# Kernel optimization log

Hardware: AMD Instinct MI355X
Metric: run time of the kernel (lower is better)

## Reference

```python
import jax, jax.numpy as jnp
import numpy as np

IN_FEATURES = 1024
OUT_FEATURES = 1024
GRID_SIZE = 5
SPLINE_ORDER = 3
GRID_RANGE = (-1.0, 1.0)


def make_grid():
    h = (GRID_RANGE[1] - GRID_RANGE[0]) / GRID_SIZE
    g = jnp.arange(-SPLINE_ORDER, GRID_SIZE + SPLINE_ORDER + 1, dtype=jnp.float32) * h + GRID_RANGE[0]
    return jnp.tile(g[None, :], (IN_FEATURES, 1))  # (in, G + 2k + 1)


def b_splines(x, grid):
    # x: (N, in), grid: (in, G+2k+1) -> bases: (N, in, G+k)
    xe = x[..., None]
    bases = ((xe >= grid[:, :-1]) & (xe < grid[:, 1:])).astype(x.dtype)
    for k in range(1, SPLINE_ORDER + 1):
        left = (xe - grid[:, :-(k + 1)]) / (grid[:, k:-1] - grid[:, :-(k + 1)])
        right = (grid[:, k + 1:] - xe) / (grid[:, k + 1:] - grid[:, 1:-k])
        bases = left * bases[:, :, :-1] + right * bases[:, :, 1:]
    return bases


def setup_inputs() -> dict:
    key = jax.random.key(0)
    k1, k2, k3 = jax.random.split(key, 3)
    x = jax.random.uniform(k1, (8192, IN_FEATURES), dtype=jnp.float32)
    # lecun_normal-style init: std = 1/sqrt(fan_in)
    base_weight = jax.random.normal(k2, (OUT_FEATURES, IN_FEATURES), dtype=jnp.float32) / np.sqrt(IN_FEATURES)
    coeff = GRID_SIZE + SPLINE_ORDER
    spline_weight = jax.random.normal(k3, (OUT_FEATURES, IN_FEATURES, coeff), dtype=jnp.float32) / np.sqrt(IN_FEATURES * coeff)
    spline_scaler = jnp.ones((OUT_FEATURES, IN_FEATURES), dtype=jnp.float32)
    grid = make_grid()
    return {"x": x, "grid": grid, "base_weight": base_weight,
            "spline_weight": spline_weight, "spline_scaler": spline_scaler}


def reference(x, grid, base_weight, spline_weight, spline_scaler):
    N = x.shape[0]
    base_out = jax.nn.silu(x) @ base_weight.T  # (N, out)
    bases = b_splines(x, grid)                 # (N, in, G+k)
    scaled_sw = spline_weight * spline_scaler[..., None]  # (out, in, G+k)
    spline_out = bases.reshape(N, -1) @ scaled_sw.reshape(OUT_FEATURES, -1).T  # (N, out)
    return base_out + spline_out
```

## Files before the change

### kernel.cpp

```cpp
#include <hip/hip_runtime.h>
#include <hip/hip_bf16.h>

#define IN_F 1024
#define OUT_F 1024
#define KTOT (IN_F * 9)
#define M_ROWS 8192

#define BK 64
#define NT (KTOT / BK)
#define NT_H (NT / 2)

#define A_TILE_E 16384
#define B_TILE_E 8192

typedef short bf16x8 __attribute__((ext_vector_type(8)));
typedef int   i32x4  __attribute__((ext_vector_type(4)));
typedef float f32x4  __attribute__((ext_vector_type(4)));

#define AS1 __attribute__((address_space(1)))
#define AS3 __attribute__((address_space(3)))

__device__ __forceinline__ void kan_basis_fast(
    float xv, const float* __restrict__ g,
    const float* __restrict__ inv1, const float* __restrict__ inv2,
    const float* __restrict__ inv3, float* __restrict__ out) {
  float b[11];
#pragma unroll
  for (int j = 0; j < 11; ++j)
    b[j] = (xv >= g[j] && xv < g[j + 1]) ? 1.0f : 0.0f;
#pragma unroll
  for (int j = 0; j < 10; ++j)
    b[j] = (xv - g[j]) * inv1[j] * b[j] + (g[j + 2] - xv) * inv1[j + 1] * b[j + 1];
#pragma unroll
  for (int j = 0; j < 9; ++j)
    b[j] = (xv - g[j]) * inv2[j] * b[j] + (g[j + 3] - xv) * inv2[j + 1] * b[j + 1];
#pragma unroll
  for (int j = 0; j < 8; ++j)
    b[j] = (xv - g[j]) * inv3[j] * b[j] + (g[j + 4] - xv) * inv3[j + 1] * b[j + 1];
#pragma unroll
  for (int j = 0; j < 8; ++j) out[j] = b[j];
}

__global__ __launch_bounds__(256) void expand_a(
    const float* __restrict__ x, const float* __restrict__ grid,
    __hip_bfloat16* __restrict__ A, int row0, int nrows) {
  const int tid = threadIdx.x;
  const int lane = tid & 63;
  const int wvx = tid >> 6;
  const int l15 = lane & 15;
  const int lhi = lane >> 4;

  const int nb = blockIdx.x >> 3;
  const int ib = blockIdx.x & 7;
  const int n_l = nb * 16 + l15;
  const int i0 = ib * 128 + wvx * 32 + lhi * 8;

  const int bm = n_l >> 8, wm = (n_l >> 6) & 3, m = (n_l >> 4) & 3;

  float g[12];
  const float* gp = grid + (size_t)i0 * 12;
#pragma unroll
  for (int j = 0; j < 12; ++j) g[j] = gp[j];
  float inv1[11], inv2[10], inv3[9];
#pragma unroll
  for (int j = 0; j < 11; ++j) inv1[j] = 1.0f / (g[j + 1] - g[j]);
#pragma unroll
  for (int j = 0; j < 10; ++j) inv2[j] = 1.0f / (g[j + 2] - g[j]);
#pragma unroll
  for (int j = 0; j < 9; ++j)  inv3[j] = 1.0f / (g[j + 3] - g[j]);

  const float* xp = x + (size_t)(row0 + n_l) * IN_F + i0;
  float xs[8];
  *(f32x4*)&xs[0] = *(const f32x4*)xp;
  *(f32x4*)&xs[4] = *(const f32x4*)(xp + 4);

  bf16x8 out[9];
#pragma unroll
  for (int j = 0; j < 8; ++j) {
    float xv = xs[j];
    float bas[8];
    kan_basis_fast(xv, g, inv1, inv2, inv3, bas);
    float s = xv / (1.0f + __expf(-xv));
    out[0][j] = (short)__bfloat16_as_ushort(__float2bfloat16(s));
#pragma unroll
    for (int c = 0; c < 8; ++c)
      out[c + 1][j] = (short)__bfloat16_as_ushort(__float2bfloat16(bas[c]));
  }

#pragma unroll
  for (int c = 0; c < 9; ++c) {
    int k0 = c * IN_F + i0;
    int kt = k0 >> 6;
    int kk = (k0 >> 5) & 1;
    size_t frag = ((((size_t)bm * NT + kt) * 4 + wm) * 4 + m) * 2 + kk;
    *(bf16x8*)(A + frag * 512 + lane * 8) = out[c];
  }
}

__global__ __launch_bounds__(256) void pack_b(
    const float* __restrict__ bw, const float* __restrict__ sw,
    const float* __restrict__ sc, __hip_bfloat16* __restrict__ B) {
  const int tid = threadIdx.x;
  const int lane = tid & 63;
  const int wid = blockIdx.x * 4 + (tid >> 6);
  const int og = wid >> 5;
  const int ib32 = wid & 31;
  const int obn = og >> 3, colg = og & 7;
  const int l15 = lane & 15, lhi = lane >> 4;
  const int o = og * 16 + l15;
  const int i0 = ib32 * 32 + lhi * 8;

  float bwv[8], scv[8];
  const float* bp = bw + (size_t)o * IN_F + i0;
  const float* sp = sc + (size_t)o * IN_F + i0;
  *(f32x4*)&bwv[0] = *(const f32x4*)bp;
  *(f32x4*)&bwv[4] = *(const f32x4*)(bp + 4);
  *(f32x4*)&scv[0] = *(const f32x4*)sp;
  *(f32x4*)&scv[4] = *(const f32x4*)(sp + 4);

  bf16x8 out[9];
#pragma unroll
  for (int j = 0; j < 8; ++j) {
    out[0][j] = (short)__bfloat16_as_ushort(__float2bfloat16(bwv[j]));
    const float* swp = sw + ((size_t)o * IN_F + i0 + j) * 8;
    float swv[8];
    *(f32x4*)&swv[0] = *(const f32x4*)swp;
    *(f32x4*)&swv[4] = *(const f32x4*)(swp + 4);
#pragma unroll
    for (int c = 0; c < 8; ++c)
      out[c + 1][j] = (short)__bfloat16_as_ushort(__float2bfloat16(swv[c] * scv[j]));
  }

#pragma unroll
  for (int c = 0; c < 9; ++c) {
    int kt = c * 16 + (ib32 >> 1);
    int kk = ib32 & 1;
    size_t frag = ((size_t)obn * NT + kt) * 16 + colg * 2 + kk;
    *(bf16x8*)(B + frag * 512 + lane * 8) = out[c];
  }
}


__device__ __forceinline__ void gld16(const __hip_bfloat16* g, __hip_bfloat16* l) {
  __builtin_amdgcn_global_load_lds((AS1 void*)g, (AS3 void*)l, 16, 0, 0);
}

#define DSRO(dst, addr, IMM)                                               \
  asm volatile("ds_read_b128 %0, %1 offset:" #IMM : "=v"(dst) : "v"(addr))

#define SB __builtin_amdgcn_sched_barrier(0)

#define SLOT_E 32768
#define SLOT_B 65536

#define READ_A_KK0(d, aA) do {                                             \
    DSRO(d[0], aA, 0);     DSRO(d[1], aA, 2048);                           \
    DSRO(d[2], aA, 4096);  DSRO(d[3], aA, 6144);                           \
    DSRO(d[4], aA, 8192);  DSRO(d[5], aA, 10240);                          \
    DSRO(d[6], aA, 12288); DSRO(d[7], aA, 14336);                          \
  } while (0)
#define READ_A_KK1(d, aA) do {                                             \
    DSRO(d[0], aA, 1024);  DSRO(d[1], aA, 3072);                           \
    DSRO(d[2], aA, 5120);  DSRO(d[3], aA, 7168);                           \
    DSRO(d[4], aA, 9216);  DSRO(d[5], aA, 11264);                          \
    DSRO(d[6], aA, 13312); DSRO(d[7], aA, 15360);                          \
  } while (0)
#define READ_B_KK0(d, bA) do {                                             \
    DSRO(d[0], bA, 0);     DSRO(d[1], bA, 2048);                           \
    DSRO(d[2], bA, 4096);  DSRO(d[3], bA, 6144);                           \
  } while (0)
#define READ_B_KK1(d, bA) do {                                             \
    DSRO(d[0], bA, 1024);  DSRO(d[1], bA, 3072);                           \
    DSRO(d[2], bA, 5120);  DSRO(d[3], bA, 7168);                           \
  } while (0)

#define MFMA_B(sA, sB) do {                                                \
    __builtin_amdgcn_s_setprio(1);                                         \
    _Pragma("unroll")                                                      \
    for (int m_ = 0; m_ < 8; ++m_)                                         \
      _Pragma("unroll")                                                    \
      for (int n_ = 0; n_ < 4; ++n_)                                       \
        acc[m_][n_] = __builtin_amdgcn_mfma_f32_16x16x32_bf16(             \
            sA[m_], sB[n_], acc[m_][n_], 0, 0, 0);                         \
    __builtin_amdgcn_s_setprio(0);                                         \
  } while (0)

#define STAGE12(DST) do {                                                  \
    gld16(aGp,          (DST) + dstE);                                     \
    gld16(aGp + 4096,   (DST) + dstE + 4096);                              \
    gld16(aGp + 8192,   (DST) + dstE + 8192);                              \
    gld16(aGp + 12288,  (DST) + dstE + 12288);                             \
    gld16(bGp0,         (DST) + dstE + 16384);                             \
    gld16(bGp0 + 4096,  (DST) + dstE + 20480);                             \
    gld16(bGp1,         (DST) + dstE + 24576);                             \
    gld16(bGp1 + 4096,  (DST) + dstE + 28672);                             \
    aGp += 16384; bGp0 += 8192; bGp1 += 8192;                              \
  } while (0)

#define TILE_V12(cA, cB, nA, nB, STAGE_, READN_) do {                      \
    READ_A_KK1(ga, cA); READ_B_KK1(gb, cB);                   \
    STAGE_                                                                 \
    SB;                                                                    \
    asm volatile("s_waitcnt lgkmcnt(12)" ::: "memory"); SB;                \
    MFMA_B(fa, fb);                                                        \
    SB;                                                                    \
    asm volatile("s_waitcnt lgkmcnt(0)" ::: "memory"); SB;                 \
    asm volatile("s_waitcnt vmcnt(0)" ::: "memory"); SB;                   \
    __builtin_amdgcn_s_barrier(); SB;               \
    READN_                                                                 \
    SB;                                                                    \
    MFMA_B(ga, gb);                                                        \
    SB;                                                                    \
  } while (0)

#define READN12(nA, nB) READ_A_KK0(fa, nA); READ_B_KK0(fb, nB);

__global__ __launch_bounds__(512, 2) void gemm_v12(
    const __hip_bfloat16* __restrict__ A, const __hip_bfloat16* __restrict__ B,
    float* __restrict__ C) {
  __shared__ __align__(16) __hip_bfloat16 S[2][SLOT_E];

  const int nwg = gridDim.x;
  const int q = nwg >> 3;
  const int L = (blockIdx.x & 7) * q + (blockIdx.x >> 3);
  const int bm = L >> 3;
  const int khalf = (L >> 2) & 1;
  const int bn2 = L & 3;

  const int tid = threadIdx.x;
  const int lane = tid & 63;
  const int wv = tid >> 6;
  const int wm = wv >> 2;
  const int wn = wv & 3;
  const int l15 = lane & 15, lhi = lane >> 4;

  const int laneE = (wv * 64 + lane) * 8;
  const __hip_bfloat16* aGp =
      A + ((size_t)bm * NT + khalf * NT_H) * A_TILE_E + laneE;
  const __hip_bfloat16* bGp0 =
      B + ((size_t)(2 * bn2) * NT + khalf * NT_H) * B_TILE_E + laneE;
  const __hip_bfloat16* bGp1 =
      B + ((size_t)(2 * bn2 + 1) * NT + khalf * NT_H) * B_TILE_E + laneE;
  __hip_bfloat16* ldsP = &S[0][0];
  const int dstE = wv * 512;

  const uint32_t ldsB = (uint32_t)(uintptr_t)(AS3 const void*)&S[0][0];
  const uint32_t aA0 = ldsB + wm * 16384 + lane * 16;
  const uint32_t aA1 = aA0 + SLOT_B;
  const uint32_t bA0 = ldsB + 32768 + (wn >> 1) * 16384 + (wn & 1) * 8192 + lane * 16;
  const uint32_t bA1 = bA0 + SLOT_B;

  f32x4 acc[8][4];
#pragma unroll
  for (int m = 0; m < 8; ++m)
#pragma unroll
    for (int n = 0; n < 4; ++n) acc[m][n] = f32x4{0.f, 0.f, 0.f, 0.f};

  bf16x8 fa[8], fb[4];
  bf16x8 ga[8], gb[4];

  STAGE12(ldsP);
  asm volatile("s_waitcnt vmcnt(0)" ::: "memory");
  SB;
  __builtin_amdgcn_s_barrier();
  SB;
  READ_A_KK0(fa, aA0); READ_B_KK0(fb, bA0);
  SB;

#pragma unroll 1
  for (int tt = 0; tt < (NT_H - 2) / 2; ++tt) {
    TILE_V12(aA0, bA0, aA1, bA1, STAGE12(ldsP + SLOT_E);, READN12(aA1, bA1));
    TILE_V12(aA1, bA1, aA0, bA0, STAGE12(ldsP);,          READN12(aA0, bA0));
  }
  TILE_V12(aA0, bA0, aA1, bA1, STAGE12(ldsP + SLOT_E);, READN12(aA1, bA1));
  TILE_V12(aA1, bA1, aA0, bA0, ;, ;);

#pragma unroll
  for (int m = 0; m < 8; ++m)
#pragma unroll
    for (int n = 0; n < 4; ++n) {
      int col = bn2 * 256 + (wn >> 1) * 128 + (wn & 1) * 64 + n * 16 + l15;
      int row0 = bm * 256 + wm * 128 + m * 16 + lhi * 4;
#pragma unroll
      for (int j = 0; j < 4; ++j)
        atomicAdd(&C[(size_t)(row0 + j) * OUT_F + col], acc[m][n][j]);
    }
}

__global__ __launch_bounds__(256) void kan_naive(
    const float* __restrict__ x, const float* __restrict__ grid,
    const float* __restrict__ bw, const float* __restrict__ sw,
    const float* __restrict__ sc, float* __restrict__ out) {
  __shared__ float s_act[IN_F];
  __shared__ float s_bas[IN_F * 8];
  int n = blockIdx.x;
  for (int i = threadIdx.x; i < IN_F; i += 256) {
    float xv = x[(size_t)n * IN_F + i];
    float g[12];
    const float* gp = grid + i * 12;
#pragma unroll
    for (int t = 0; t < 12; ++t) g[t] = gp[t];
    float b[11];
#pragma unroll
    for (int j = 0; j < 11; ++j)
      b[j] = (xv >= g[j] && xv < g[j + 1]) ? 1.0f : 0.0f;
#pragma unroll
    for (int k = 1; k <= 3; ++k)
#pragma unroll
      for (int j = 0; j < 11 - k; ++j) {
        float left = (xv - g[j]) / (g[j + k] - g[j]);
        float right = (g[j + k + 1] - xv) / (g[j + k + 1] - g[j + 1]);
        b[j] = left * b[j] + right * b[j + 1];
      }
    s_act[i] = xv / (1.0f + __expf(-xv));
#pragma unroll
    for (int c = 0; c < 8; ++c) s_bas[i * 8 + c] = b[c];
  }
  __syncthreads();
  for (int o = threadIdx.x; o < OUT_F; o += 256) {
    float acc = 0.f;
    const float* bwo = bw + (size_t)o * IN_F;
    const float* swo = sw + (size_t)o * IN_F * 8;
    const float* sco = sc + (size_t)o * IN_F;
    for (int i = 0; i < IN_F; ++i) {
      acc += s_act[i] * bwo[i];
      float p = 0.f;
#pragma unroll
      for (int c = 0; c < 8; ++c) p += s_bas[i * 8 + c] * swo[i * 8 + c];
      acc += p * sco[i];
    }
    out[(size_t)n * OUT_F + o] = acc;
  }
}

extern "C" void kernel_launch(void* const* d_in, const int* in_sizes, int n_in,
                              void* d_out, int out_size, void* d_ws, size_t ws_size,
                              hipStream_t stream) {
  const float* x  = (const float*)d_in[0];
  const float* grid = (const float*)d_in[1];
  const float* bw = (const float*)d_in[2];
  const float* sw = (const float*)d_in[3];
  const float* sc = (const float*)d_in[4];
  float* out = (float*)d_out;

  const size_t Bbytes = (size_t)OUT_F * KTOT * 2;
  const size_t rowBytes = (size_t)KTOT * 2;

  if (ws_size >= Bbytes + 256 * rowBytes) {
    __hip_bfloat16* Bp = (__hip_bfloat16*)d_ws;
    __hip_bfloat16* Ap = (__hip_bfloat16*)((char*)d_ws + Bbytes);
    size_t arows = (ws_size - Bbytes) / rowBytes;
    int chunk = (int)((arows / 256) * 256);
    if (chunk > M_ROWS) chunk = M_ROWS;

    hipMemsetAsync(d_out, 0, (size_t)out_size * sizeof(float), stream);
    pack_b<<<OUT_F * 128 / 256, 256, 0, stream>>>(bw, sw, sc, Bp);
    for (int r0 = 0; r0 < M_ROWS; r0 += chunk) {
      int rows = M_ROWS - r0 < chunk ? M_ROWS - r0 : chunk;
      expand_a<<<(rows / 16) * 8, 256, 0, stream>>>(x, grid, Ap, r0, rows);
      gemm_v12<<<(rows / 256) * 8, 512, 0, stream>>>(Ap, Bp, out + (size_t)r0 * OUT_F);
    }
  } else {
    kan_naive<<<M_ROWS, 256, 0, stream>>>(x, grid, bw, sw, sc, out);
  }
}
```

Baseline: 217.4 us.

## Switch GEMM to four-slot half-tile LDS ring with deeper prefetch

The bf16 MFMA GEMM moves from two double-buffered full BK=64 slots to four 32 KB slots, each holding half a K tile (one kk sub-step). Each body stages the next-next sub-tile with global_load_lds, waits only for older loads (vmcnt(4)), then barriers and reads the next fragments while running MFMAs on the current ones. The aim is to keep global-load latency hidden two steps ahead and to shrink the work done per barrier. The cost is twice as many barriers per K tile and more intricate index and offset bookkeeping across the unrolled loop.

```diff
diff --git a/kernel.cpp b/kernel.cpp
--- a/kernel.cpp
+++ b/kernel.cpp
@@ -150,31 +150,18 @@
 
 #define SB __builtin_amdgcn_sched_barrier(0)
 
-#define SLOT_E 32768
-#define SLOT_B 65536
-
-#define READ_A_KK0(d, aA) do {                                             \
-    DSRO(d[0], aA, 0);     DSRO(d[1], aA, 2048);                           \
-    DSRO(d[2], aA, 4096);  DSRO(d[3], aA, 6144);                           \
-    DSRO(d[4], aA, 8192);  DSRO(d[5], aA, 10240);                          \
-    DSRO(d[6], aA, 12288); DSRO(d[7], aA, 14336);                          \
-  } while (0)
-#define READ_A_KK1(d, aA) do {                                             \
-    DSRO(d[0], aA, 1024);  DSRO(d[1], aA, 3072);                           \
-    DSRO(d[2], aA, 5120);  DSRO(d[3], aA, 7168);                           \
-    DSRO(d[4], aA, 9216);  DSRO(d[5], aA, 11264);                          \
-    DSRO(d[6], aA, 13312); DSRO(d[7], aA, 15360);                          \
-  } while (0)
-#define READ_B_KK0(d, bA) do {                                             \
-    DSRO(d[0], bA, 0);     DSRO(d[1], bA, 2048);                           \
-    DSRO(d[2], bA, 4096);  DSRO(d[3], bA, 6144);                           \
-  } while (0)
-#define READ_B_KK1(d, bA) do {                                             \
-    DSRO(d[0], bA, 1024);  DSRO(d[1], bA, 3072);                           \
-    DSRO(d[2], bA, 5120);  DSRO(d[3], bA, 7168);                           \
-  } while (0)
-
-#define MFMA_B(sA, sB) do {                                                \
+#define READ_A8(d, aA) do {                                                \
+    DSRO(d[0], aA, 0);     DSRO(d[1], aA, 1024);                           \
+    DSRO(d[2], aA, 2048);  DSRO(d[3], aA, 3072);                           \
+    DSRO(d[4], aA, 4096);  DSRO(d[5], aA, 5120);                           \
+    DSRO(d[6], aA, 6144);  DSRO(d[7], aA, 7168);                           \
+  } while (0)
+#define READ_B4(d, bA) do {                                                \
+    DSRO(d[0], bA, 0);     DSRO(d[1], bA, 1024);                           \
+    DSRO(d[2], bA, 2048);  DSRO(d[3], bA, 3072);                           \
+  } while (0)
+
+#define MFMA32(sA, sB) do {                                                \
     __builtin_amdgcn_s_setprio(1);                                         \
     _Pragma("unroll")                                                      \
     for (int m_ = 0; m_ < 8; ++m_)                                         \
@@ -185,40 +172,38 @@
     __builtin_amdgcn_s_setprio(0);                                         \
   } while (0)
 
-#define STAGE12(DST) do {                                                  \
-    gld16(aGp,          (DST) + dstE);                                     \
-    gld16(aGp + 4096,   (DST) + dstE + 4096);                              \
-    gld16(aGp + 8192,   (DST) + dstE + 8192);                              \
-    gld16(aGp + 12288,  (DST) + dstE + 12288);                             \
-    gld16(bGp0,         (DST) + dstE + 16384);                             \
-    gld16(bGp0 + 4096,  (DST) + dstE + 20480);                             \
-    gld16(bGp1,         (DST) + dstE + 24576);                             \
-    gld16(bGp1 + 4096,  (DST) + dstE + 28672);                             \
-    aGp += 16384; bGp0 += 8192; bGp1 += 8192;                              \
-  } while (0)
-
-#define TILE_V12(cA, cB, nA, nB, STAGE_, READN_) do {                      \
-    READ_A_KK1(ga, cA); READ_B_KK1(gb, cB);                   \
-    STAGE_                                                                 \
-    SB;                                                                    \
-    asm volatile("s_waitcnt lgkmcnt(12)" ::: "memory"); SB;                \
-    MFMA_B(fa, fb);                                                        \
-    SB;                                                                    \
-    asm volatile("s_waitcnt lgkmcnt(0)" ::: "memory"); SB;                 \
-    asm volatile("s_waitcnt vmcnt(0)" ::: "memory"); SB;                   \
-    __builtin_amdgcn_s_barrier(); SB;               \
-    READN_                                                                 \
-    SB;                                                                    \
-    MFMA_B(ga, gb);                                                        \
-    SB;                                                                    \
-  } while (0)
-
-#define READN12(nA, nB) READ_A_KK0(fa, nA); READ_B_KK0(fb, nB);
-
-__global__ __launch_bounds__(512, 2) void gemm_v12(
+#define STAGE13(SLOT, GA_, GB_) do {                                       \
+    __hip_bfloat16* d_ = ldsP + (SLOT) * 16384;                            \
+    gld16(aPw + (GA_),         d_ + wv * 512);                             \
+    gld16(aPw + (GA_) + 8192,  d_ + 4096 + wv * 512);                      \
+    gld16(bP0w + (GB_),        d_ + 8192 + wv * 512);                      \
+    gld16(bP1w + (GB_),        d_ + 12288 + wv * 512);                     \
+  } while (0)
+
+#define VM4 asm volatile("s_waitcnt vmcnt(4)" ::: "memory")
+#define VM0 asm volatile("s_waitcnt vmcnt(0)" ::: "memory")
+#define LGK0 asm volatile("s_waitcnt lgkmcnt(0)" ::: "memory")
+
+#define BODY13(FA, FB, GA, GB, SN, STAGE_, VMW_) do {                      \
+    STAGE_;                                                                \
+    SB;                                                                    \
+    VMW_;                                                                  \
+    SB;                                                                    \
+    LGK0;                                                                  \
+    SB;                                                                    \
+    __builtin_amdgcn_s_barrier();                                          \
+    SB;                                                                    \
+    READ_A8(GA, aRdB + (SN) * 32768u);                                     \
+    READ_B4(GB, bRdB + (SN) * 32768u);                                     \
+    SB;                                                                    \
+    MFMA32(FA, FB);                                                        \
+    SB;                                                                    \
+  } while (0)
+
+__global__ __launch_bounds__(512, 2) void gemm_v13(
     const __hip_bfloat16* __restrict__ A, const __hip_bfloat16* __restrict__ B,
     float* __restrict__ C) {
-  __shared__ __align__(16) __hip_bfloat16 S[2][SLOT_E];
+  __shared__ __align__(16) __hip_bfloat16 S[4][16384];
 
   const int nwg = gridDim.x;
   const int q = nwg >> 3;
@@ -234,21 +219,17 @@
   const int wn = wv & 3;
   const int l15 = lane & 15, lhi = lane >> 4;
 
-  const int laneE = (wv * 64 + lane) * 8;
-  const __hip_bfloat16* aGp =
-      A + ((size_t)bm * NT + khalf * NT_H) * A_TILE_E + laneE;
-  const __hip_bfloat16* bGp0 =
-      B + ((size_t)(2 * bn2) * NT + khalf * NT_H) * B_TILE_E + laneE;
-  const __hip_bfloat16* bGp1 =
-      B + ((size_t)(2 * bn2 + 1) * NT + khalf * NT_H) * B_TILE_E + laneE;
+  const __hip_bfloat16* aPw =
+      A + ((size_t)bm * NT + khalf * NT_H) * A_TILE_E + wv * 1024 + lane * 8;
+  const __hip_bfloat16* bP0w =
+      B + ((size_t)(2 * bn2) * NT + khalf * NT_H) * B_TILE_E + wv * 1024 + lane * 8;
+  const __hip_bfloat16* bP1w =
+      B + ((size_t)(2 * bn2 + 1) * NT + khalf * NT_H) * B_TILE_E + wv * 1024 + lane * 8;
   __hip_bfloat16* ldsP = &S[0][0];
-  const int dstE = wv * 512;
 
   const uint32_t ldsB = (uint32_t)(uintptr_t)(AS3 const void*)&S[0][0];
-  const uint32_t aA0 = ldsB + wm * 16384 + lane * 16;
-  const uint32_t aA1 = aA0 + SLOT_B;
-  const uint32_t bA0 = ldsB + 32768 + (wn >> 1) * 16384 + (wn & 1) * 8192 + lane * 16;
-  const uint32_t bA1 = bA0 + SLOT_B;
+  const uint32_t aRdB = ldsB + wm * 8192 + lane * 16;
+  const uint32_t bRdB = ldsB + 16384 + wn * 4096 + lane * 16;
 
   f32x4 acc[8][4];
 #pragma unroll
@@ -259,27 +240,37 @@
   bf16x8 fa[8], fb[4];
   bf16x8 ga[8], gb[4];
 
-  STAGE12(ldsP);
-  asm volatile("s_waitcnt vmcnt(0)" ::: "memory");
+  STAGE13(0, 0, 0);
+  STAGE13(1, 512, 512);
+  VM4;
   SB;
   __builtin_amdgcn_s_barrier();
   SB;
-  READ_A_KK0(fa, aA0); READ_B_KK0(fb, bA0);
+  READ_A8(fa, aRdB);
+  READ_B4(fb, bRdB);
   SB;
+  aPw += 16384; bP0w += 8192; bP1w += 8192;
 
 #pragma unroll 1
-  for (int tt = 0; tt < (NT_H - 2) / 2; ++tt) {
-    TILE_V12(aA0, bA0, aA1, bA1, STAGE12(ldsP + SLOT_E);, READN12(aA1, bA1));
-    TILE_V12(aA1, bA1, aA0, bA0, STAGE12(ldsP);,          READN12(aA0, bA0));
-  }
-  TILE_V12(aA0, bA0, aA1, bA1, STAGE12(ldsP + SLOT_E);, READN12(aA1, bA1));
-  TILE_V12(aA1, bA1, aA0, bA0, ;, ;);
+  for (int tt = 0; tt < 35; ++tt) {
+    BODY13(fa, fb, ga, gb, 1, STAGE13(2, 0, 0), VM4);
+    BODY13(ga, gb, fa, fb, 2, STAGE13(3, 512, 512), VM4);
+    BODY13(fa, fb, ga, gb, 3, STAGE13(0, 16384, 8192), VM4);
+    BODY13(ga, gb, fa, fb, 0, STAGE13(1, 16896, 8704), VM4);
+    aPw += 32768; bP0w += 16384; bP1w += 16384;
+  }
+  BODY13(fa, fb, ga, gb, 1, STAGE13(2, 0, 0), VM4);
+  BODY13(ga, gb, fa, fb, 2, STAGE13(3, 512, 512), VM4);
+  BODY13(fa, fb, ga, gb, 3, ;, VM0);
+  LGK0;
+  SB;
+  MFMA32(ga, gb);
 
 #pragma unroll
   for (int m = 0; m < 8; ++m)
 #pragma unroll
     for (int n = 0; n < 4; ++n) {
-      int col = bn2 * 256 + (wn >> 1) * 128 + (wn & 1) * 64 + n * 16 + l15;
+      int col = bn2 * 256 + wn * 64 + n * 16 + l15;
       int row0 = bm * 256 + wm * 128 + m * 16 + lhi * 4;
 #pragma unroll
       for (int j = 0; j < 4; ++j)
@@ -358,7 +349,7 @@
     for (int r0 = 0; r0 < M_ROWS; r0 += chunk) {
       int rows = M_ROWS - r0 < chunk ? M_ROWS - r0 : chunk;
       expand_a<<<(rows / 16) * 8, 256, 0, stream>>>(x, grid, Ap, r0, rows);
-      gemm_v12<<<(rows / 256) * 8, 512, 0, stream>>>(Ap, Bp, out + (size_t)r0 * OUT_F);
+      gemm_v13<<<(rows / 256) * 8, 512, 0, stream>>>(Ap, Bp, out + (size_t)r0 * OUT_F);
     }
   } else {
     kan_naive<<<M_ROWS, 256, 0, stream>>>(x, grid, bw, sw, sc, out);
```

Measured after the change: 217.8 us. No clear change (+0.2%).
